# Optimization experiments

Hardware: AMD Instinct MI355X
Metric: run time of the kernel (lower is better)

## Reference

```python
import jax, jax.numpy as jnp
import numpy as np

HEADS = 8

def _rotate_every_two(t):
    # t: [..., d]; interleaved rotation (-x2, x1) pairs
    x1 = t[..., ::2]
    x2 = t[..., 1::2]
    return jnp.stack([-x2, x1], axis=-1).reshape(t.shape)

def _theta_shift(t, sin, cos):
    return t * cos + _rotate_every_two(t) * sin

def setup_inputs() -> dict:
    key = jax.random.key(0)
    ks = jax.random.split(key, 5)
    B, H, W, C = 4, 40, 40, 512
    dh = C // HEADS
    x = jax.random.normal(ks[0], (B, H, W, C), dtype=jnp.float32)
    sin = jax.random.normal(ks[1], (H, W, dh), dtype=jnp.float32)
    cos = jax.random.normal(ks[2], (H, W, dh), dtype=jnp.float32)
    # 1x1 conv weight [3C, C] (kernel dims squeezed) + bias
    w_qkv = jax.random.normal(ks[3], (3 * C, C), dtype=jnp.float32) * (C ** -0.5)
    b_qkv = jnp.zeros((3 * C,), dtype=jnp.float32)
    return {"x": x, "sin": sin, "cos": cos, "w_qkv": w_qkv, "b_qkv": b_qkv}

def reference(x, sin, cos, w_qkv, b_qkv):
    B, H, W, C = x.shape
    heads = HEADS
    dh = C // heads
    scale = dh ** -0.5
    # 1x1 conv == per-pixel linear projection
    qkv = jnp.einsum('bhwc,oc->bhwo', x, w_qkv) + b_qkv  # [B,H,W,3C]
    q, k, v = jnp.split(qkv, 3, axis=-1)

    def to_heads(t):
        # channel order is (heads, dim_head) per the torch rearrange
        return t.reshape(B, H, W, heads, dh).transpose(0, 3, 1, 2, 4)  # [B,heads,H,W,dh]

    q = _theta_shift(to_heads(q), sin, cos)
    k = _theta_shift(to_heads(k), sin, cos)
    # v is computed but unused downstream in the original module (bug preserved)

    N = H * W
    q = q.reshape(B, heads, N, dh)
    k = k.reshape(B, heads, N, dh)

    attn = jnp.einsum('bhnd,bhmd->bhnm', q, k) * scale  # [B,heads,N,N]
    p = jax.nn.softmax(attn, axis=-1)
    # NOTE: original code does matmul(logist, kfine_heads) — K, not V. Kept faithful.
    out = jnp.einsum('bhnm,bhmd->bhnd', p, k)  # [B,heads,N,dh]
    out = out.transpose(0, 2, 1, 3).reshape(B, H, W, C)
    return out
```

## Files before the change

### kernel.cpp

```cpp
#include <hip/hip_runtime.h>
#include <hip/hip_bf16.h>


typedef __hip_bfloat16 bf16;
typedef __attribute__((ext_vector_type(8))) short short8;
typedef __attribute__((ext_vector_type(4))) short bfx4;
typedef __attribute__((ext_vector_type(4))) float f32x4;

#define NSP 1600
#define CDIM 512
#define DH 64

__device__ __forceinline__ f32x4 mfma32(short8 a, short8 b, f32x4 c) {
  return __builtin_amdgcn_mfma_f32_16x16x32_bf16(a, b, c, 0, 0, 0);
}

#if __has_builtin(__builtin_amdgcn_mfma_f32_16x16x16bf16_1k)
__device__ __forceinline__ f32x4 mfma_k16(bfx4 a, bfx4 b, f32x4 c) {
  return __builtin_amdgcn_mfma_f32_16x16x16bf16_1k(a, b, c, 0, 0, 0);
}
#else
__device__ __forceinline__ f32x4 mfma_k16(bfx4 a, bfx4 b, f32x4 c) {
  short8 a8 = {a.x, a.y, a.z, a.w, 0, 0, 0, 0};
  short8 b8 = {b.x, b.y, b.z, b.w, 0, 0, 0, 0};
  return __builtin_amdgcn_mfma_f32_16x16x32_bf16(a8, b8, c, 0, 0, 0);
}
#endif

__device__ __forceinline__ short8 cvt8(float4 v0, float4 v1) {
  short8 r; bf16* p = (bf16*)&r;
  p[0] = __float2bfloat16(v0.x); p[1] = __float2bfloat16(v0.y);
  p[2] = __float2bfloat16(v0.z); p[3] = __float2bfloat16(v0.w);
  p[4] = __float2bfloat16(v1.x); p[5] = __float2bfloat16(v1.y);
  p[6] = __float2bfloat16(v1.z); p[7] = __float2bfloat16(v1.w);
  return r;
}

extern "C" __global__ __launch_bounds__(256)
void cvt_kernel(const float* __restrict__ x, const float* __restrict__ w,
                const float* __restrict__ sin_t, const float* __restrict__ cos_t,
                bf16* __restrict__ x_bf, bf16* __restrict__ w_bf,
                float* __restrict__ sinT, float* __restrict__ cosT)
{
  __shared__ float t_lds[64][68];
  const int bid = blockIdx.x, tid = threadIdx.x;
  if (bid < 1600) {
    const size_t i = (size_t)bid * 2048 + tid * 8;
    float4 v0 = *(const float4*)(x + i);
    float4 v1 = *(const float4*)(x + i + 4);
    *(short8*)(x_bf + i) = cvt8(v0, v1);
  } else if (bid < 1856) {
    const size_t i = (size_t)(bid - 1600) * 2048 + tid * 8;
    float4 v0 = *(const float4*)(w + i);
    float4 v1 = *(const float4*)(w + i + 4);
    *(short8*)(w_bf + i) = cvt8(v0, v1);
  } else {
    const int t = bid - 1856;
    const float* src = (t < 25) ? sin_t : cos_t;
    float* dst = (t < 25) ? sinT : cosT;
    const int nt = (t < 25) ? t : t - 25;
    const int r = tid >> 2, c = (tid & 3) * 16;
#pragma unroll
    for (int j = 0; j < 4; ++j)
      *(float4*)&t_lds[r][c + j * 4] =
          *(const float4*)(src + (size_t)(nt * 64 + r) * 64 + c + j * 4);
    __syncthreads();
#pragma unroll
    for (int j4 = 0; j4 < 4; ++j4) {
      float4 o;
      o.x = t_lds[c + j4 * 4 + 0][r];
      o.y = t_lds[c + j4 * 4 + 1][r];
      o.z = t_lds[c + j4 * 4 + 2][r];
      o.w = t_lds[c + j4 * 4 + 3][r];
      *(float4*)(dst + (size_t)r * NSP + nt * 64 + c + j4 * 4) = o;
    }
  }
}

extern "C" __global__ __launch_bounds__(256)
void proj_kernel(const bf16* __restrict__ x_bf, const bf16* __restrict__ w_bf,
                 const float* __restrict__ bias, const float* __restrict__ sinT,
                 const float* __restrict__ cosT, bf16* __restrict__ q_ws,
                 bf16* __restrict__ k_ws, bf16* __restrict__ kT_ws)
{
  __shared__ __align__(16) char smem[36864];
  bf16 (*x_lds)[72] = (bf16(*)[72])smem;
  bf16 (*w_lds)[72] = (bf16(*)[72])(smem + 18432);
  bf16* ep = (bf16*)smem;

  const int tid  = threadIdx.x;
  const int wave = tid >> 6;
  const int lane = tid & 63;
  const int col  = lane & 15;
  const int quad = lane >> 4;
  const int wm = wave >> 1, wo = wave & 1;
  const int m0 = blockIdx.x * 128;
  const int o0 = blockIdx.y * 128;

  f32x4 acc[4][4];
#pragma unroll
  for (int i = 0; i < 4; ++i)
#pragma unroll
    for (int j = 0; j < 4; ++j) acc[i][j] = {0.f, 0.f, 0.f, 0.f};

  const int srow = tid >> 1;
  const int sch  = (tid & 1) * 32;

  for (int kt = 0; kt < 8; ++kt) {
    __syncthreads();
    {
      const bf16* xs = x_bf + (size_t)(m0 + srow) * CDIM + kt * 64 + sch;
      const bf16* ws = w_bf + (size_t)(o0 + srow) * CDIM + kt * 64 + sch;
#pragma unroll
      for (int j = 0; j < 4; ++j) {
        *(short8*)&x_lds[srow][sch + j * 8] = *(const short8*)(xs + j * 8);
        *(short8*)&w_lds[srow][sch + j * 8] = *(const short8*)(ws + j * 8);
      }
    }
    __syncthreads();
#pragma unroll
    for (int half = 0; half < 2; ++half) {
      short8 af[4], bfr[4];
#pragma unroll
      for (int mt = 0; mt < 4; ++mt)
        af[mt] = *(short8*)&x_lds[wm * 64 + mt * 16 + col][half * 32 + quad * 8];
#pragma unroll
      for (int ot = 0; ot < 4; ++ot)
        bfr[ot] = *(short8*)&w_lds[wo * 64 + ot * 16 + col][half * 32 + quad * 8];
#pragma unroll
      for (int mt = 0; mt < 4; ++mt)
#pragma unroll
        for (int ot = 0; ot < 4; ++ot)
          acc[mt][ot] = mfma32(af[mt], bfr[ot], acc[mt][ot]);
    }
  }

  __syncthreads();
  const int b_idx = (m0 + wm * 64) / NSP;
  const int n0w   = m0 + wm * 64 - b_idx * NSP;
  const bool isq  = (o0 < 512);
#pragma unroll
  for (int ot = 0; ot < 4; ++ot) {
    const int o_local = wo * 64 + ot * 16 + col;
    const int o_g = o0 + o_local;
    const float bv = bias[o_g];
    const int d = o_g & 63;
#pragma unroll
    for (int mt = 0; mt < 4; ++mt) {
      const int nl = mt * 16 + quad * 4;
      float t[4], rot[4];
#pragma unroll
      for (int r = 0; r < 4; ++r) t[r] = acc[mt][ot][r] + bv;
#pragma unroll
      for (int r = 0; r < 4; ++r) {
        float tp = __shfl_xor(t[r], 1, 64);
        rot[r] = (lane & 1) ? tp : -tp;
      }
      const float4 c4 = *(const float4*)(cosT + (size_t)d * NSP + n0w + nl);
      const float4 s4 = *(const float4*)(sinT + (size_t)d * NSP + n0w + nl);
      float res[4];
      res[0] = t[0] * c4.x + rot[0] * s4.x;
      res[1] = t[1] * c4.y + rot[1] * s4.y;
      res[2] = t[2] * c4.z + rot[2] * s4.z;
      res[3] = t[3] * c4.w + rot[3] * s4.w;
      if (isq) {
#pragma unroll
        for (int r = 0; r < 4; ++r) res[r] *= 0.125f;
      }
      bfx4 pk; bf16* pp = (bf16*)&pk;
#pragma unroll
      for (int r = 0; r < 4; ++r) pp[r] = __float2bfloat16(res[r]);
      *(bfx4*)&ep[o_local * 132 + wm * 64 + nl] = pk;
    }
  }
  __syncthreads();

  if (isq) {
    const int m_l = tid >> 1, half = tid & 1;
    const int gm = m0 + m_l;
    const int bi = gm / NSP, n = gm - bi * NSP;
    const int h = (o0 >> 6) + half;
    bf16* base = q_ws + ((size_t)(bi * 8 + h) * NSP + n) * 64;
#pragma unroll
    for (int c = 0; c < 8; ++c) {
      short8 v; bf16* vp = (bf16*)&v;
#pragma unroll
      for (int j = 0; j < 8; ++j) vp[j] = ep[(half * 64 + c * 8 + j) * 132 + m_l];
      *(short8*)(base + c * 8) = v;
    }
  } else {
    {
      const int m_l = tid >> 1, half = tid & 1;
      const int gm = m0 + m_l;
      const int bi = gm / NSP, n = gm - bi * NSP;
      const int h = ((o0 - 512) >> 6) + half;
      bf16* base = k_ws + ((size_t)(bi * 8 + h) * NSP + n) * 64;
#pragma unroll
      for (int c = 0; c < 8; ++c) {
        short8 v; bf16* vp = (bf16*)&v;
#pragma unroll
        for (int j = 0; j < 8; ++j) vp[j] = ep[(half * 64 + c * 8 + j) * 132 + m_l];
        *(short8*)(base + c * 8) = v;
      }
    }
    {
      const int half2 = tid >> 7, d = (tid >> 1) & 63, T = tid & 1;
      const int gmb = m0 + T * 64;
      const int bi2 = gmb / NSP, ktile = (gmb - bi2 * NSP) >> 6;
      const int h2 = ((o0 - 512) >> 6) + half2;
      bf16* base = kT_ws + ((size_t)(bi2 * 8 + h2) * 64 + d) * NSP + ktile * 64;
      const bf16* eprow = ep + (half2 * 64 + d) * 132 + T * 64;
#pragma unroll
      for (int cc = 0; cc < 8; ++cc) {
        const int K2 = cc >> 2, q = cc & 3;
        short8 v;
        ((bfx4*)&v)[0] = *(const bfx4*)(eprow + K2 * 32 + q * 4);
        ((bfx4*)&v)[1] = *(const bfx4*)(eprow + K2 * 32 + 16 + q * 4);
        *(short8*)(base + cc * 8) = v;
      }
    }
  }
}

extern "C" __global__ __launch_bounds__(256)
void attn_kernel(const bf16* __restrict__ q_ws, const bf16* __restrict__ k_ws,
                 const bf16* __restrict__ kT_ws, float* __restrict__ out)
{
  __shared__ __align__(16) char smem[36864];
  bf16 (*k_lds)[64][72]  = (bf16(*)[64][72])smem;
  bf16 (*kT_lds)[64][72] = (bf16(*)[64][72])(smem + 18432);
  float (*red)[64][36]   = (float(*)[64][36])smem;

  const int qt = blockIdx.x, bh = blockIdx.y;
  const int b = bh >> 3, h = bh & 7;
  const int tid  = threadIdx.x;
  const int wave = tid >> 6;
  const int lane = tid & 63;
  const int col  = lane & 15;
  const int quad = lane >> 4;
  const int qg = wave & 1, kh = wave >> 1;

  short8 qb[2][2];
#pragma unroll
  for (int ct = 0; ct < 2; ++ct) {
    const bf16* qp =
        q_ws + ((size_t)bh * NSP + qt * 64 + (qg * 2 + ct) * 16 + col) * 64;
    qb[ct][0] = *(const short8*)(qp + quad * 8);
    qb[ct][1] = *(const short8*)(qp + 32 + quad * 8);
  }

  f32x4 oacc[4][2];
#pragma unroll
  for (int i = 0; i < 4; ++i)
#pragma unroll
    for (int j = 0; j < 2; ++j) oacc[i][j] = {0.f, 0.f, 0.f, 0.f};
  float l_part[2] = {0.f, 0.f};

  const bf16* kp  = k_ws  + (size_t)bh * NSP * 64;
  const bf16* ktp = kT_ws + (size_t)bh * 64 * NSP;
  const int sr = tid >> 2, sc = (tid & 3) * 16;

#define ATTN_STAGE(BUF, KT)                                                    \
  {                                                                            \
    const bf16* s1 = kp + (size_t)((KT) * 64 + sr) * 64 + sc;                  \
    *(short8*)&k_lds[BUF][sr][sc]      = *(const short8*)s1;                   \
    *(short8*)&k_lds[BUF][sr][sc + 8]  = *(const short8*)(s1 + 8);             \
    const bf16* s2 = ktp + (size_t)sr * NSP + (KT) * 64 + sc;                  \
    *(short8*)&kT_lds[BUF][sr][sc]     = *(const short8*)s2;                   \
    *(short8*)&kT_lds[BUF][sr][sc + 8] = *(const short8*)(s2 + 8);             \
  }

  ATTN_STAGE(0, 0)

  for (int kt = 0; kt < 25; ++kt) {
    __syncthreads();
    const int cur = kt & 1;
    if (kt + 1 < 25) ATTN_STAGE(cur ^ 1, kt + 1)

    f32x4 s[2][2];
#pragma unroll
    for (int ti = 0; ti < 2; ++ti) {
      const int row = (2 * kh + ti) * 16 + col;
      short8 a0 = *(short8*)&k_lds[cur][row][quad * 8];
      short8 a1 = *(short8*)&k_lds[cur][row][32 + quad * 8];
#pragma unroll
      for (int ct = 0; ct < 2; ++ct) {
        f32x4 t = {0.f, 0.f, 0.f, 0.f};
        t = mfma32(a0, qb[ct][0], t);
        t = mfma32(a1, qb[ct][1], t);
        s[ti][ct] = t;
      }
    }

    bfx4 p4[2][2];
#pragma unroll
    for (int ti = 0; ti < 2; ++ti)
#pragma unroll
      for (int ct = 0; ct < 2; ++ct) {
#pragma unroll
        for (int r = 0; r < 4; ++r) s[ti][ct][r] = __expf(s[ti][ct][r]);
        l_part[ct] += s[ti][ct][0] + s[ti][ct][1] + s[ti][ct][2] + s[ti][ct][3];
        bf16* pp = (bf16*)&p4[ti][ct];
#pragma unroll
        for (int r = 0; r < 4; ++r) pp[r] = __float2bfloat16(s[ti][ct][r]);
      }

#pragma unroll
    for (int dt = 0; dt < 4; ++dt) {
      short8 a8 = *(short8*)&kT_lds[cur][dt * 16 + col][(kh * 4 + quad) * 8];
      bfx4 alo = __builtin_shufflevector(a8, a8, 0, 1, 2, 3);
      bfx4 ahi = __builtin_shufflevector(a8, a8, 4, 5, 6, 7);
#pragma unroll
      for (int ct = 0; ct < 2; ++ct) {
        oacc[dt][ct] = mfma_k16(alo, p4[0][ct], oacc[dt][ct]);
        oacc[dt][ct] = mfma_k16(ahi, p4[1][ct], oacc[dt][ct]);
      }
    }
  }

#pragma unroll
  for (int ct = 0; ct < 2; ++ct) {
    l_part[ct] += __shfl_xor(l_part[ct], 16, 64);
    l_part[ct] += __shfl_xor(l_part[ct], 32, 64);
  }

  __syncthreads();
  if (wave >= 2) {
    float* dst = &red[wave - 2][lane][0];
#pragma unroll
    for (int dt = 0; dt < 4; ++dt)
#pragma unroll
      for (int ct = 0; ct < 2; ++ct)
        *(f32x4*)(dst + (dt * 2 + ct) * 4) = oacc[dt][ct];
    dst[32] = l_part[0]; dst[33] = l_part[1];
  }
  __syncthreads();
  if (wave < 2) {
    const float* srcr = &red[wave][lane][0];
#pragma unroll
    for (int dt = 0; dt < 4; ++dt)
#pragma unroll
      for (int ct = 0; ct < 2; ++ct)
        oacc[dt][ct] += *(const f32x4*)(srcr + (dt * 2 + ct) * 4);
    const float inv0 = 1.f / (l_part[0] + srcr[32]);
    const float inv1 = 1.f / (l_part[1] + srcr[33]);
#pragma unroll
    for (int ct = 0; ct < 2; ++ct) {
      const float inv = ct ? inv1 : inv0;
      const int qrow = qt * 64 + (qg * 2 + ct) * 16 + col;
      float* ob = out + ((size_t)b * NSP + qrow) * CDIM + h * 64;
#pragma unroll
      for (int dt = 0; dt < 4; ++dt) {
        float4 v;
        v.x = oacc[dt][ct][0] * inv; v.y = oacc[dt][ct][1] * inv;
        v.z = oacc[dt][ct][2] * inv; v.w = oacc[dt][ct][3] * inv;
        *(float4*)(ob + dt * 16 + quad * 4) = v;
      }
    }
  }
}

extern "C" void kernel_launch(void* const* d_in, const int* in_sizes, int n_in,
                              void* d_out, int out_size, void* d_ws, size_t ws_size,
                              hipStream_t stream) {
  const float* x     = (const float*)d_in[0];
  const float* sin_t = (const float*)d_in[1];
  const float* cos_t = (const float*)d_in[2];
  const float* w_qkv = (const float*)d_in[3];
  const float* b_qkv = (const float*)d_in[4];
  float* out = (float*)d_out;

  const size_t QK = (size_t)32 * NSP * DH;
  bf16* q_ws  = (bf16*)d_ws;
  bf16* k_ws  = q_ws + QK;
  bf16* kT_ws = k_ws + QK;
  bf16* x_bf  = kT_ws + QK;
  bf16* w_bf  = x_bf + (size_t)6400 * CDIM;
  float* sinT = (float*)(w_bf + (size_t)1024 * CDIM);
  float* cosT = sinT + (size_t)DH * NSP;

  cvt_kernel<<<1906, 256, 0, stream>>>(x, w_qkv, sin_t, cos_t, x_bf, w_bf, sinT, cosT);

  dim3 gproj(50, 8);
  proj_kernel<<<gproj, 256, 0, stream>>>(x_bf, w_bf, b_qkv, sinT, cosT,
                                         q_ws, k_ws, kT_ws);

  dim3 gattn(25, 32);
  attn_kernel<<<gattn, 256, 0, stream>>>(q_ws, k_ws, kT_ws, out);
}
```

Measured before the change: 149.8 us.

## Store K in MFMA fragment order and load fragments directly from global

The projection kernel now writes K and K-transpose into a per-tile layout that matches the MFMA operand fragments lane by lane. The attention kernel then loads each fragment with one coalesced 16-byte global load per lane, with no LDS staging, no double buffering and no per-iteration barriers. This removes LDS traffic and synchronisation from the inner loop and cuts LDS use, which may raise occupancy. In exchange the loads go to global memory or L2 with no software prefetch, so latency may become exposed, and each K tile is re-read by all 25 query-tile blocks.

```diff
diff --git a/kernel.cpp b/kernel.cpp
--- a/kernel.cpp
+++ b/kernel.cpp
@@ -81,7 +81,7 @@
 void proj_kernel(const bf16* __restrict__ x_bf, const bf16* __restrict__ w_bf,
                  const float* __restrict__ bias, const float* __restrict__ sinT,
                  const float* __restrict__ cosT, bf16* __restrict__ q_ws,
-                 bf16* __restrict__ k_ws, bf16* __restrict__ kT_ws)
+                 bf16* __restrict__ k2_ws, bf16* __restrict__ kt2_ws)
 {
   __shared__ __align__(16) char smem[36864];
   bf16 (*x_lds)[72] = (bf16(*)[72])smem;
@@ -189,47 +189,47 @@
       *(short8*)(base + c * 8) = v;
     }
   } else {
-    {
-      const int m_l = tid >> 1, half = tid & 1;
-      const int gm = m0 + m_l;
-      const int bi = gm / NSP, n = gm - bi * NSP;
-      const int h = ((o0 - 512) >> 6) + half;
-      bf16* base = k_ws + ((size_t)(bi * 8 + h) * NSP + n) * 64;
-#pragma unroll
-      for (int c = 0; c < 8; ++c) {
-        short8 v; bf16* vp = (bf16*)&v;
-#pragma unroll
-        for (int j = 0; j < 8; ++j) vp[j] = ep[(half * 64 + c * 8 + j) * 132 + m_l];
-        *(short8*)(base + c * 8) = v;
-      }
-    }
-    {
-      const int half2 = tid >> 7, d = (tid >> 1) & 63, T = tid & 1;
+    const int h0 = (o0 - 512) >> 6;
+#pragma unroll
+    for (int it = 0; it < 8; ++it) {
+      const int ci = it * 256 + tid;
+      const int hh = ci >> 10, T = (ci >> 9) & 1, inner = ci & 511;
+      const int ccol = inner & 15, cq = (inner >> 4) & 3;
+      const int f = (inner >> 6) & 1, ti = (inner >> 7) & 1, kh2 = (inner >> 8) & 1;
       const int gmb = m0 + T * 64;
-      const int bi2 = gmb / NSP, ktile = (gmb - bi2 * NSP) >> 6;
-      const int h2 = ((o0 - 512) >> 6) + half2;
-      bf16* base = kT_ws + ((size_t)(bi2 * 8 + h2) * 64 + d) * NSP + ktile * 64;
-      const bf16* eprow = ep + (half2 * 64 + d) * 132 + T * 64;
-#pragma unroll
-      for (int cc = 0; cc < 8; ++cc) {
-        const int K2 = cc >> 2, q = cc & 3;
-        short8 v;
-        ((bfx4*)&v)[0] = *(const bfx4*)(eprow + K2 * 32 + q * 4);
-        ((bfx4*)&v)[1] = *(const bfx4*)(eprow + K2 * 32 + 16 + q * 4);
-        *(short8*)(base + cc * 8) = v;
-      }
+      const int bi = gmb / NSP, ktile = (gmb - bi * NSP) >> 6;
+      const int m_l = T * 64 + (2 * kh2 + ti) * 16 + ccol;
+      const int er0 = hh * 64 + (f * 4 + cq) * 8;
+      short8 v; bf16* vp = (bf16*)&v;
+#pragma unroll
+      for (int j = 0; j < 8; ++j) vp[j] = ep[(er0 + j) * 132 + m_l];
+      *(short8*)(k2_ws +
+          (((size_t)(bi * 8 + h0 + hh) * 25 + ktile) * 512 + inner) * 8) = v;
+    }
+#pragma unroll
+    for (int it = 0; it < 8; ++it) {
+      const int ci = it * 256 + tid;
+      const int hh = ci >> 10, T = (ci >> 9) & 1, inner = ci & 511;
+      const int ccol = inner & 15, cq = (inner >> 4) & 3;
+      const int dt = (inner >> 6) & 3, kh2 = (inner >> 8) & 1;
+      const int gmb = m0 + T * 64;
+      const int bi = gmb / NSP, ktile = (gmb - bi * NSP) >> 6;
+      const bf16* eprow =
+          ep + (hh * 64 + dt * 16 + ccol) * 132 + T * 64 + kh2 * 32 + cq * 4;
+      short8 v;
+      ((bfx4*)&v)[0] = *(const bfx4*)(eprow);
+      ((bfx4*)&v)[1] = *(const bfx4*)(eprow + 16);
+      *(short8*)(kt2_ws +
+          (((size_t)(bi * 8 + h0 + hh) * 25 + ktile) * 512 + inner) * 8) = v;
     }
   }
 }
 
 extern "C" __global__ __launch_bounds__(256)
-void attn_kernel(const bf16* __restrict__ q_ws, const bf16* __restrict__ k_ws,
-                 const bf16* __restrict__ kT_ws, float* __restrict__ out)
+void attn_kernel(const bf16* __restrict__ q_ws, const bf16* __restrict__ k2_ws,
+                 const bf16* __restrict__ kt2_ws, float* __restrict__ out)
 {
-  __shared__ __align__(16) char smem[36864];
-  bf16 (*k_lds)[64][72]  = (bf16(*)[64][72])smem;
-  bf16 (*kT_lds)[64][72] = (bf16(*)[64][72])(smem + 18432);
-  float (*red)[64][36]   = (float(*)[64][36])smem;
+  __shared__ float red[2][64][36];
 
   const int qt = blockIdx.x, bh = blockIdx.y;
   const int b = bh >> 3, h = bh & 7;
@@ -256,41 +256,35 @@
     for (int j = 0; j < 2; ++j) oacc[i][j] = {0.f, 0.f, 0.f, 0.f};
   float l_part[2] = {0.f, 0.f};
 
-  const bf16* kp  = k_ws  + (size_t)bh * NSP * 64;
-  const bf16* ktp = kT_ws + (size_t)bh * 64 * NSP;
-  const int sr = tid >> 2, sc = (tid & 3) * 16;
-
-#define ATTN_STAGE(BUF, KT)                                                    \
-  {                                                                            \
-    const bf16* s1 = kp + (size_t)((KT) * 64 + sr) * 64 + sc;                  \
-    *(short8*)&k_lds[BUF][sr][sc]      = *(const short8*)s1;                   \
-    *(short8*)&k_lds[BUF][sr][sc + 8]  = *(const short8*)(s1 + 8);             \
-    const bf16* s2 = ktp + (size_t)sr * NSP + (KT) * 64 + sc;                  \
-    *(short8*)&kT_lds[BUF][sr][sc]     = *(const short8*)s2;                   \
-    *(short8*)&kT_lds[BUF][sr][sc + 8] = *(const short8*)(s2 + 8);             \
-  }
-
-  ATTN_STAGE(0, 0)
+  const bf16* k2b  = k2_ws  + (size_t)bh * 25 * 4096;
+  const bf16* kt2b = kt2_ws + (size_t)bh * 25 * 4096;
 
   for (int kt = 0; kt < 25; ++kt) {
-    __syncthreads();
-    const int cur = kt & 1;
-    if (kt + 1 < 25) ATTN_STAGE(cur ^ 1, kt + 1)
+    const bf16* kc  = k2b  + kt * 4096;
+    const bf16* kc2 = kt2b + kt * 4096;
+
+    short8 kf[2][2];
+#pragma unroll
+    for (int ti = 0; ti < 2; ++ti)
+#pragma unroll
+      for (int f = 0; f < 2; ++f)
+        kf[ti][f] =
+            *(const short8*)(kc + (((kh * 2 + ti) * 2 + f) * 64 + lane) * 8);
+    short8 ktf[4];
+#pragma unroll
+    for (int dt = 0; dt < 4; ++dt)
+      ktf[dt] = *(const short8*)(kc2 + ((kh * 4 + dt) * 64 + lane) * 8);
 
     f32x4 s[2][2];
 #pragma unroll
-    for (int ti = 0; ti < 2; ++ti) {
-      const int row = (2 * kh + ti) * 16 + col;
-      short8 a0 = *(short8*)&k_lds[cur][row][quad * 8];
-      short8 a1 = *(short8*)&k_lds[cur][row][32 + quad * 8];
+    for (int ti = 0; ti < 2; ++ti)
 #pragma unroll
       for (int ct = 0; ct < 2; ++ct) {
         f32x4 t = {0.f, 0.f, 0.f, 0.f};
-        t = mfma32(a0, qb[ct][0], t);
-        t = mfma32(a1, qb[ct][1], t);
+        t = mfma32(kf[ti][0], qb[ct][0], t);
+        t = mfma32(kf[ti][1], qb[ct][1], t);
         s[ti][ct] = t;
       }
-    }
 
     bfx4 p4[2][2];
 #pragma unroll
@@ -307,9 +301,8 @@
 
 #pragma unroll
     for (int dt = 0; dt < 4; ++dt) {
-      short8 a8 = *(short8*)&kT_lds[cur][dt * 16 + col][(kh * 4 + quad) * 8];
-      bfx4 alo = __builtin_shufflevector(a8, a8, 0, 1, 2, 3);
-      bfx4 ahi = __builtin_shufflevector(a8, a8, 4, 5, 6, 7);
+      bfx4 alo = __builtin_shufflevector(ktf[dt], ktf[dt], 0, 1, 2, 3);
+      bfx4 ahi = __builtin_shufflevector(ktf[dt], ktf[dt], 4, 5, 6, 7);
 #pragma unroll
       for (int ct = 0; ct < 2; ++ct) {
         oacc[dt][ct] = mfma_k16(alo, p4[0][ct], oacc[dt][ct]);
@@ -324,7 +317,6 @@
     l_part[ct] += __shfl_xor(l_part[ct], 32, 64);
   }
 
-  __syncthreads();
   if (wave >= 2) {
     float* dst = &red[wave - 2][lane][0];
 #pragma unroll
@@ -371,20 +363,20 @@
   float* out = (float*)d_out;
 
   const size_t QK = (size_t)32 * NSP * DH;
-  bf16* q_ws  = (bf16*)d_ws;
-  bf16* k_ws  = q_ws + QK;
-  bf16* kT_ws = k_ws + QK;
-  bf16* x_bf  = kT_ws + QK;
-  bf16* w_bf  = x_bf + (size_t)6400 * CDIM;
-  float* sinT = (float*)(w_bf + (size_t)1024 * CDIM);
-  float* cosT = sinT + (size_t)DH * NSP;
+  bf16* q_ws   = (bf16*)d_ws;
+  bf16* k2_ws  = q_ws + QK;
+  bf16* kt2_ws = k2_ws + QK;
+  bf16* x_bf   = kt2_ws + QK;
+  bf16* w_bf   = x_bf + (size_t)6400 * CDIM;
+  float* sinT  = (float*)(w_bf + (size_t)1024 * CDIM);
+  float* cosT  = sinT + (size_t)DH * NSP;
 
   cvt_kernel<<<1906, 256, 0, stream>>>(x, w_qkv, sin_t, cos_t, x_bf, w_bf, sinT, cosT);
 
   dim3 gproj(50, 8);
   proj_kernel<<<gproj, 256, 0, stream>>>(x_bf, w_bf, b_qkv, sinT, cosT,
-                                         q_ws, k_ws, kT_ws);
+                                         q_ws, k2_ws, kt2_ws);
 
   dim3 gattn(25, 32);
-  attn_kernel<<<gattn, 256, 0, stream>>>(q_ws, k_ws, kT_ws, out);
-}
+  attn_kernel<<<gattn, 256, 0, stream>>>(q_ws, k2_ws, kt2_ws, out);
+}
```

New measurement: 140.5 us. -6.2%, faster.
